# Kernel tuning notes

Hardware: AMD Instinct MI355X
Metric: run time of the kernel (lower is better)

## Reference

```python
import jax, jax.numpy as jnp
import numpy as np

N = 100000
NNZ = 3200000
NFEAT, NHID, NCLASS = 512, 256, 41

def setup_inputs() -> dict:
    key = jax.random.key(0)
    ks = jax.random.split(key, 8)
    x = jax.random.normal(ks[0], (N, NFEAT), dtype=jnp.float32)
    adj_rows = jnp.sort(jax.random.randint(ks[1], (NNZ,), 0, N))
    adj_cols = jax.random.randint(ks[2], (NNZ,), 0, N)
    adj_vals = jax.random.uniform(ks[3], (NNZ,), dtype=jnp.float32) / 32.0  # ~normalized adj
    s1 = 1.0 / np.sqrt(NHID)
    s2 = 1.0 / np.sqrt(NCLASS)
    w1 = jax.random.uniform(ks[4], (NFEAT, NHID), minval=-s1, maxval=s1, dtype=jnp.float32)
    b1 = jax.random.uniform(ks[5], (NHID,), minval=-s1, maxval=s1, dtype=jnp.float32)
    w2 = jax.random.uniform(ks[6], (NHID, NCLASS), minval=-s2, maxval=s2, dtype=jnp.float32)
    b2 = jax.random.uniform(ks[7], (NCLASS,), minval=-s2, maxval=s2, dtype=jnp.float32)
    return {"x": x, "adj_rows": adj_rows, "adj_cols": adj_cols, "adj_vals": adj_vals,
            "w1": w1, "b1": b1, "w2": w2, "b2": b2}

def spmm(rows, cols, vals, dense):
    # sparse [N,N] @ dense [N,D] via gather + segment_sum
    gathered = dense[cols] * vals[:, None]  # [nnz, D]
    return jax.ops.segment_sum(gathered, rows, num_segments=N)

def reference(x, adj_rows, adj_cols, adj_vals, w1, b1, w2, b2):
    # layer 1: A(XW) + b, relu  (GraphConvolution)
    h = spmm(adj_rows, adj_cols, adj_vals, x @ w1) + b1
    h = jax.nn.relu(h)
    # dropout: inference mode (training=False) -> identity
    # layer 2: (AX)W + b  (GraphConvolution2)
    out = spmm(adj_rows, adj_cols, adj_vals, h) @ w2 + b2
    return jax.nn.log_softmax(out, axis=1)
```

## Files before the change

kernel.cpp:

```cpp
#include <hip/hip_runtime.h>
#include <math.h>

#define N_NODES 100000
#define NNZ_E   3200000
#define NFEAT   512
#define NHID    256
#define NCLASS  41
#define NC_PAD  48
#define P_STRIDE 64

typedef __attribute__((ext_vector_type(8))) short   short8;
typedef __attribute__((ext_vector_type(8))) unsigned short ushort8;
typedef __attribute__((ext_vector_type(4))) float   f32x4;
typedef __attribute__((ext_vector_type(2))) float   f32x2;

__device__ __forceinline__ unsigned short f2bf(float f) {
    unsigned u = __builtin_bit_cast(unsigned, f);
    unsigned r = u + 0x7fffu + ((u >> 16) & 1u);
    return (unsigned short)(r >> 16);
}
__device__ __forceinline__ unsigned char f2fp8(float f) {
    return (unsigned char)(__builtin_amdgcn_cvt_pk_fp8_f32(f, 0.f, 0, false) & 0xff);
}

__global__ void prep_w_kernel(const float* __restrict__ w1, const float* __restrict__ w2,
                              unsigned short* __restrict__ w1t, unsigned short* __restrict__ w2t) {
    int tid = blockIdx.x * 256 + threadIdx.x;
    if (tid < NHID * NFEAT) {
        int n = tid >> 9, k = tid & 511;
        w1t[tid] = f2bf(w1[k * NHID + n]);
    }
    int t2 = tid - NHID * NFEAT;
    if (t2 >= 0 && t2 < NC_PAD * NHID) {
        int n = t2 >> 8, k = t2 & 255;
        w2t[t2] = (n < NCLASS) ? f2bf(w2[k * NCLASS + n]) : (unsigned short)0;
    }
}

__global__ void rowptr_kernel(const int* __restrict__ rows, int* __restrict__ row_ptr) {
    int r = blockIdx.x * 256 + threadIdx.x;
    if (r > N_NODES) return;
    int lo = 0, hi = NNZ_E;
    while (lo < hi) {
        int mid = (lo + hi) >> 1;
        if (rows[mid] < r) lo = mid + 1; else hi = mid;
    }
    row_ptr[r] = lo;
}

__global__ __launch_bounds__(256) void gemm1_kernel(const float* __restrict__ x,
                                                    const unsigned short* __restrict__ w1t,
                                                    unsigned char* __restrict__ xw) {
    const int rb   = blockIdx.x * 64;
    const int wave = threadIdx.x >> 6;
    const int lane = threadIdx.x & 63;
    const int l15  = lane & 15;
    const int quad = lane >> 4;

    f32x4 acc[4][4] = {};

    const float* arow_ptr[4];
#pragma unroll
    for (int mt = 0; mt < 4; mt++) {
        int r = rb + mt * 16 + l15;
        if (r >= N_NODES) r = N_NODES - 1;
        arow_ptr[mt] = x + (long)r * NFEAT + quad * 8;
    }
    const unsigned short* brow = w1t + (long)(wave * 64 + l15) * NFEAT + quad * 8;

    for (int kc = 0; kc < NFEAT; kc += 32) {
        short8 a[4];
#pragma unroll
        for (int mt = 0; mt < 4; mt++) {
            float4 f0 = *(const float4*)(arow_ptr[mt] + kc);
            float4 f1 = *(const float4*)(arow_ptr[mt] + kc + 4);
            ushort8 v;
            v[0] = f2bf(f0.x); v[1] = f2bf(f0.y); v[2] = f2bf(f0.z); v[3] = f2bf(f0.w);
            v[4] = f2bf(f1.x); v[5] = f2bf(f1.y); v[6] = f2bf(f1.z); v[7] = f2bf(f1.w);
            a[mt] = __builtin_bit_cast(short8, v);
        }
#pragma unroll
        for (int nt = 0; nt < 4; nt++) {
            short8 b = *(const short8*)(brow + (long)nt * 16 * NFEAT + kc);
#pragma unroll
            for (int mt = 0; mt < 4; mt++)
                acc[mt][nt] = __builtin_amdgcn_mfma_f32_16x16x32_bf16(a[mt], b, acc[mt][nt], 0, 0, 0);
        }
    }

#pragma unroll
    for (int mt = 0; mt < 4; mt++) {
#pragma unroll
        for (int nt = 0; nt < 4; nt++) {
            int col = wave * 64 + nt * 16 + l15;
#pragma unroll
            for (int r = 0; r < 4; r++) {
                int row = rb + mt * 16 + quad * 4 + r;
                if (row < N_NODES)
                    xw[(long)row * NHID + col] = f2fp8(acc[mt][nt][r]);
            }
        }
    }
}

__global__ __launch_bounds__(256) void spmm1_kernel(const unsigned char* __restrict__ xw,
                                                    const int* __restrict__ row_ptr,
                                                    const int* __restrict__ cols,
                                                    const float* __restrict__ vals,
                                                    const float* __restrict__ b1,
                                                    unsigned short* __restrict__ h) {
    int row = blockIdx.x * 4 + (threadIdx.x >> 6);
    if (row >= N_NODES) return;
    int lane = threadIdx.x & 63;
    int e0 = row_ptr[row], e1 = row_ptr[row + 1];

    float a0 = 0.f, a1 = 0.f, a2 = 0.f, a3 = 0.f;
    for (int base = e0; base < e1; base += 64) {
        int   myc = 0;
        float myv = 0.f;
        int idx = base + lane;
        if (idx < e1) { myc = cols[idx]; myv = vals[idx]; }
        int cnt = e1 - base; if (cnt > 64) cnt = 64;
        int j = 0;
        for (; j + 8 <= cnt; j += 8) {
            int c[8]; float v[8];
#pragma unroll
            for (int u = 0; u < 8; u++) { c[u] = __shfl(myc, j + u); v[u] = __shfl(myv, j + u); }
            unsigned q[8];
#pragma unroll
            for (int u = 0; u < 8; u++) q[u] = *(const unsigned*)(xw + (long)c[u] * NHID + lane * 4);
#pragma unroll
            for (int u = 0; u < 8; u++) {
                f32x2 lo = __builtin_amdgcn_cvt_pk_f32_fp8((int)q[u], false);
                f32x2 hi = __builtin_amdgcn_cvt_pk_f32_fp8((int)q[u], true);
                a0 += v[u] * lo[0];
                a1 += v[u] * lo[1];
                a2 += v[u] * hi[0];
                a3 += v[u] * hi[1];
            }
        }
        for (; j < cnt; j++) {
            int   c = __shfl(myc, j);
            float v = __shfl(myv, j);
            unsigned q = *(const unsigned*)(xw + (long)c * NHID + lane * 4);
            f32x2 lo = __builtin_amdgcn_cvt_pk_f32_fp8((int)q, false);
            f32x2 hi = __builtin_amdgcn_cvt_pk_f32_fp8((int)q, true);
            a0 += v * lo[0];
            a1 += v * lo[1];
            a2 += v * hi[0];
            a3 += v * hi[1];
        }
    }
    float4 bv = *(const float4*)(b1 + lane * 4);
    a0 = fmaxf(a0 + bv.x, 0.f);
    a1 = fmaxf(a1 + bv.y, 0.f);
    a2 = fmaxf(a2 + bv.z, 0.f);
    a3 = fmaxf(a3 + bv.w, 0.f);
    uint2 o;
    o.x = (unsigned)f2bf(a0) | ((unsigned)f2bf(a1) << 16);
    o.y = (unsigned)f2bf(a2) | ((unsigned)f2bf(a3) << 16);
    *(uint2*)(h + (long)row * NHID + lane * 4) = o;
}

__global__ __launch_bounds__(256) void gemm2_kernel(const unsigned short* __restrict__ h,
                                                    const unsigned short* __restrict__ w2t,
                                                    unsigned char* __restrict__ p) {
    int rt = blockIdx.x * 4 + (threadIdx.x >> 6);
    int row0 = rt * 16;
    if (row0 >= N_NODES) return;
    int lane = threadIdx.x & 63;
    int l15 = lane & 15, quad = lane >> 4;

    int arow = row0 + l15; if (arow >= N_NODES) arow = N_NODES - 1;
    f32x4 acc[3] = {};
#pragma unroll
    for (int kc = 0; kc < NHID; kc += 32) {
        short8 a = *(const short8*)(h + (long)arow * NHID + kc + quad * 8);
#pragma unroll
        for (int nt = 0; nt < 3; nt++) {
            short8 b = *(const short8*)(w2t + (long)(nt * 16 + l15) * NHID + kc + quad * 8);
            acc[nt] = __builtin_amdgcn_mfma_f32_16x16x32_bf16(a, b, acc[nt], 0, 0, 0);
        }
    }
#pragma unroll
    for (int nt = 0; nt < 3; nt++) {
        int col = nt * 16 + l15;
#pragma unroll
        for (int r = 0; r < 4; r++) {
            int row = row0 + quad * 4 + r;
            if (row < N_NODES)
                p[(long)row * P_STRIDE + col] = f2fp8(acc[nt][r]);
        }
    }
}

__global__ __launch_bounds__(256) void spmm2_kernel(const unsigned char* __restrict__ p,
                                                    const int* __restrict__ row_ptr,
                                                    const int* __restrict__ cols,
                                                    const float* __restrict__ vals,
                                                    const float* __restrict__ b2,
                                                    float* __restrict__ out) {
    int row = blockIdx.x * 4 + (threadIdx.x >> 6);
    if (row >= N_NODES) return;
    int lane = threadIdx.x & 63;
    int e = lane >> 5;
    int t = lane & 31;
    int e0 = row_ptr[row], e1 = row_ptr[row + 1];

    float a0 = 0.f, a1 = 0.f, a2 = 0.f, a3 = 0.f;
    for (int base = e0; base < e1; base += 64) {
        int   myc = 0;
        float myv = 0.f;
        int idx = base + lane;
        if (idx < e1) { myc = cols[idx]; myv = vals[idx]; }
        int cnt = e1 - base; if (cnt > 64) cnt = 64;
        int j = 0;
        for (; j + 8 <= cnt; j += 8) {
            int c[4]; float v[4];
#pragma unroll
            for (int u = 0; u < 4; u++) {
                c[u] = __shfl(myc, j + 2 * u + e);
                v[u] = __shfl(myv, j + 2 * u + e);
            }
            unsigned q[4];
#pragma unroll
            for (int u = 0; u < 4; u++)
                q[u] = (t < 12) ? *(const unsigned*)(p + (long)c[u] * P_STRIDE + 4 * t) : 0u;
#pragma unroll
            for (int u = 0; u < 4; u++) {
                f32x2 lo = __builtin_amdgcn_cvt_pk_f32_fp8((int)q[u], false);
                f32x2 hi = __builtin_amdgcn_cvt_pk_f32_fp8((int)q[u], true);
                a0 += v[u] * lo[0];
                a1 += v[u] * lo[1];
                a2 += v[u] * hi[0];
                a3 += v[u] * hi[1];
            }
        }
        for (; j < cnt; j += 2) {
            int jj = j + e;
            int jc = jj < cnt ? jj : cnt - 1;
            int   c = __shfl(myc, jc);
            float v = __shfl(myv, jc);
            if (jj >= cnt) v = 0.f;
            unsigned q = (t < 12) ? *(const unsigned*)(p + (long)c * P_STRIDE + 4 * t) : 0u;
            f32x2 lo = __builtin_amdgcn_cvt_pk_f32_fp8((int)q, false);
            f32x2 hi = __builtin_amdgcn_cvt_pk_f32_fp8((int)q, true);
            a0 += v * lo[0];
            a1 += v * lo[1];
            a2 += v * hi[0];
            a3 += v * hi[1];
        }
    }
    a0 += __shfl_xor(a0, 32);
    a1 += __shfl_xor(a1, 32);
    a2 += __shfl_xor(a2, 32);
    a3 += __shfl_xor(a3, 32);

    int c0 = 4 * t, c1 = 4 * t + 1, c2 = 4 * t + 2, c3 = 4 * t + 3;
    float l0 = (c0 < NCLASS) ? a0 + b2[c0] : -__builtin_inff();
    float l1 = (c1 < NCLASS) ? a1 + b2[c1] : -__builtin_inff();
    float l2 = (c2 < NCLASS) ? a2 + b2[c2] : -__builtin_inff();
    float l3 = (c3 < NCLASS) ? a3 + b2[c3] : -__builtin_inff();
    float m = fmaxf(fmaxf(l0, l1), fmaxf(l2, l3));
#pragma unroll
    for (int s = 16; s; s >>= 1) m = fmaxf(m, __shfl_xor(m, s));
    float esum = ((c0 < NCLASS) ? __expf(l0 - m) : 0.f)
               + ((c1 < NCLASS) ? __expf(l1 - m) : 0.f)
               + ((c2 < NCLASS) ? __expf(l2 - m) : 0.f)
               + ((c3 < NCLASS) ? __expf(l3 - m) : 0.f);
#pragma unroll
    for (int s = 16; s; s >>= 1) esum += __shfl_xor(esum, s);
    float lse = m + __logf(esum);
    if (e == 0) {
        long ob = (long)row * NCLASS;
        if (c0 < NCLASS) out[ob + c0] = l0 - lse;
        if (c1 < NCLASS) out[ob + c1] = l1 - lse;
        if (c2 < NCLASS) out[ob + c2] = l2 - lse;
        if (c3 < NCLASS) out[ob + c3] = l3 - lse;
    }
}

extern "C" void kernel_launch(void* const* d_in, const int* in_sizes, int n_in,
                              void* d_out, int out_size, void* d_ws, size_t ws_size,
                              hipStream_t stream) {
    const float* x        = (const float*)d_in[0];
    const int*   adj_rows = (const int*)  d_in[1];
    const int*   adj_cols = (const int*)  d_in[2];
    const float* adj_vals = (const float*)d_in[3];
    const float* w1       = (const float*)d_in[4];
    const float* b1       = (const float*)d_in[5];
    const float* w2       = (const float*)d_in[6];
    const float* b2       = (const float*)d_in[7];
    float* out = (float*)d_out;

    char* ws = (char*)d_ws;
    unsigned short* w1t     = (unsigned short*)(ws);
    unsigned short* w2t     = (unsigned short*)(ws + 0x40000);
    int*            row_ptr = (int*)           (ws + 0x46000);
    unsigned char*  xw      = (unsigned char*) (ws + 0xA8000);
    unsigned short* hbuf    = (unsigned short*)(ws + 0xA8000 + 25600000L);
    unsigned char*  p       = (unsigned char*) (ws + 0xA8000);

    prep_w_kernel<<<(NHID * NFEAT + NC_PAD * NHID + 255) / 256, 256, 0, stream>>>(w1, w2, w1t, w2t);
    rowptr_kernel<<<(N_NODES + 1 + 255) / 256, 256, 0, stream>>>(adj_rows, row_ptr);
    gemm1_kernel<<<(N_NODES + 63) / 64, 256, 0, stream>>>(x, w1t, xw);
    spmm1_kernel<<<(N_NODES + 3) / 4, 256, 0, stream>>>(xw, row_ptr, adj_cols, adj_vals, b1, hbuf);
    gemm2_kernel<<<((N_NODES + 15) / 16 + 3) / 4, 256, 0, stream>>>(hbuf, w2t, p);
    spmm2_kernel<<<(N_NODES + 3) / 4, 256, 0, stream>>>(p, row_ptr, adj_cols, adj_vals, b2, out);
}
```

Baseline: 634.3 us.

## Quantize x and W1 to FP8 and tile GEMM1 through LDS with FP8 MFMA

Adds a pre-pass that converts x to FP8 and stores W1 transposed as FP8. GEMM1 now uses 128x128 tiles staged through swizzled LDS with direct global-to-LDS loads, and FP8 MFMA in place of BF16. The goal is fewer bytes read in the GEMM and faster MFMA throughput. The trade-off is an extra full pass over x (read 200MB fp32, write 50MB), lower precision on the first-layer inputs, and a reshuffled workspace layout.

```diff
diff --git a/kernel.cpp b/kernel.cpp
--- a/kernel.cpp
+++ b/kernel.cpp
@@ -14,6 +14,9 @@
 typedef __attribute__((ext_vector_type(4))) float   f32x4;
 typedef __attribute__((ext_vector_type(2))) float   f32x2;
 
+typedef __attribute__((address_space(1))) const unsigned int gu32;
+typedef __attribute__((address_space(3))) unsigned int lu32;
+
 __device__ __forceinline__ unsigned short f2bf(float f) {
     unsigned u = __builtin_bit_cast(unsigned, f);
     unsigned r = u + 0x7fffu + ((u >> 16) & 1u);
@@ -23,12 +26,31 @@
     return (unsigned char)(__builtin_amdgcn_cvt_pk_fp8_f32(f, 0.f, 0, false) & 0xff);
 }
 
+__global__ __launch_bounds__(256) void prep_x_kernel(const float* __restrict__ x,
+                                                     unsigned char* __restrict__ xq) {
+    long i = (long)(blockIdx.x * 256 + threadIdx.x) * 16;
+    float4 f0 = *(const float4*)(x + i);
+    float4 f1 = *(const float4*)(x + i + 4);
+    float4 f2 = *(const float4*)(x + i + 8);
+    float4 f3 = *(const float4*)(x + i + 12);
+    uint4 o;
+    o.x = (unsigned)__builtin_amdgcn_cvt_pk_fp8_f32(f0.x, f0.y, 0, false);
+    o.x = (unsigned)__builtin_amdgcn_cvt_pk_fp8_f32(f0.z, f0.w, (int)o.x, true);
+    o.y = (unsigned)__builtin_amdgcn_cvt_pk_fp8_f32(f1.x, f1.y, 0, false);
+    o.y = (unsigned)__builtin_amdgcn_cvt_pk_fp8_f32(f1.z, f1.w, (int)o.y, true);
+    o.z = (unsigned)__builtin_amdgcn_cvt_pk_fp8_f32(f2.x, f2.y, 0, false);
+    o.z = (unsigned)__builtin_amdgcn_cvt_pk_fp8_f32(f2.z, f2.w, (int)o.z, true);
+    o.w = (unsigned)__builtin_amdgcn_cvt_pk_fp8_f32(f3.x, f3.y, 0, false);
+    o.w = (unsigned)__builtin_amdgcn_cvt_pk_fp8_f32(f3.z, f3.w, (int)o.w, true);
+    *(uint4*)(xq + i) = o;
+}
+
 __global__ void prep_w_kernel(const float* __restrict__ w1, const float* __restrict__ w2,
-                              unsigned short* __restrict__ w1t, unsigned short* __restrict__ w2t) {
+                              unsigned char* __restrict__ w1q, unsigned short* __restrict__ w2t) {
     int tid = blockIdx.x * 256 + threadIdx.x;
     if (tid < NHID * NFEAT) {
         int n = tid >> 9, k = tid & 511;
-        w1t[tid] = f2bf(w1[k * NHID + n]);
+        w1q[tid] = f2fp8(w1[k * NHID + n]);
     }
     int t2 = tid - NHID * NFEAT;
     if (t2 >= 0 && t2 < NC_PAD * NHID) {
@@ -48,54 +70,78 @@
     row_ptr[r] = lo;
 }
 
-__global__ __launch_bounds__(256) void gemm1_kernel(const float* __restrict__ x,
-                                                    const unsigned short* __restrict__ w1t,
+__global__ __launch_bounds__(256) void gemm1_kernel(const unsigned char* __restrict__ xq,
+                                                    const unsigned char* __restrict__ w1q,
                                                     unsigned char* __restrict__ xw) {
-    const int rb   = blockIdx.x * 64;
-    const int wave = threadIdx.x >> 6;
+    __shared__ unsigned char As[8192];
+    __shared__ unsigned char Bs[8192];
+
+    const int wv   = threadIdx.x >> 6;
     const int lane = threadIdx.x & 63;
     const int l15  = lane & 15;
     const int quad = lane >> 4;
+    const int rb   = blockIdx.x * 128;
+    const int nb   = blockIdx.y * 128;
+
+    const int srow0 = (wv * 2 + 0) * 16 + (lane >> 2);
+    const int srow1 = (wv * 2 + 1) * 16 + (lane >> 2);
+    const int g0 = (lane & 3) ^ ((srow0 >> 1) & 3);
+    const int g1 = (lane & 3) ^ ((srow1 >> 1) & 3);
+    int ga0 = rb + srow0; if (ga0 >= N_NODES) ga0 = N_NODES - 1;
+    int ga1 = rb + srow1; if (ga1 >= N_NODES) ga1 = N_NODES - 1;
+    const unsigned char* agp0 = xq + (long)ga0 * NFEAT + g0 * 16;
+    const unsigned char* agp1 = xq + (long)ga1 * NFEAT + g1 * 16;
+    const unsigned char* bgp0 = w1q + (long)(nb + srow0) * NFEAT + g0 * 16;
+    const unsigned char* bgp1 = w1q + (long)(nb + srow1) * NFEAT + g1 * 16;
 
     f32x4 acc[4][4] = {};
 
-    const float* arow_ptr[4];
+    for (int kc = 0; kc < NFEAT; kc += 64) {
+        __builtin_amdgcn_global_load_lds((gu32*)(agp0 + kc), (lu32*)(As + (wv * 2 + 0) * 1024), 16, 0, 0);
+        __builtin_amdgcn_global_load_lds((gu32*)(agp1 + kc), (lu32*)(As + (wv * 2 + 1) * 1024), 16, 0, 0);
+        __builtin_amdgcn_global_load_lds((gu32*)(bgp0 + kc), (lu32*)(Bs + (wv * 2 + 0) * 1024), 16, 0, 0);
+        __builtin_amdgcn_global_load_lds((gu32*)(bgp1 + kc), (lu32*)(Bs + (wv * 2 + 1) * 1024), 16, 0, 0);
+        __syncthreads();
+
+        unsigned long long a[4][2], b[4][2];
+#pragma unroll
+        for (int mt = 0; mt < 4; mt++) {
+            int row = (wv & 1) * 64 + mt * 16 + l15;
+#pragma unroll
+            for (int ks = 0; ks < 2; ks++) {
+                int p8 = (ks * 4 + quad) ^ (row & 6);
+                a[mt][ks] = *(const unsigned long long*)(As + row * 64 + p8 * 8);
+            }
+        }
+#pragma unroll
+        for (int nt = 0; nt < 4; nt++) {
+            int nr = (wv >> 1) * 64 + nt * 16 + l15;
+#pragma unroll
+            for (int ks = 0; ks < 2; ks++) {
+                int p8 = (ks * 4 + quad) ^ (nr & 6);
+                b[nt][ks] = *(const unsigned long long*)(Bs + nr * 64 + p8 * 8);
+            }
+        }
+#pragma unroll
+        for (int ks = 0; ks < 2; ks++)
+#pragma unroll
+            for (int nt = 0; nt < 4; nt++)
+#pragma unroll
+                for (int mt = 0; mt < 4; mt++)
+                    acc[mt][nt] = __builtin_amdgcn_mfma_f32_16x16x32_fp8_fp8(
+                        (long)a[mt][ks], (long)b[nt][ks], acc[mt][nt], 0, 0, 0);
+        __syncthreads();
+    }
+
 #pragma unroll
     for (int mt = 0; mt < 4; mt++) {
-        int r = rb + mt * 16 + l15;
-        if (r >= N_NODES) r = N_NODES - 1;
-        arow_ptr[mt] = x + (long)r * NFEAT + quad * 8;
-    }
-    const unsigned short* brow = w1t + (long)(wave * 64 + l15) * NFEAT + quad * 8;
-
-    for (int kc = 0; kc < NFEAT; kc += 32) {
-        short8 a[4];
-#pragma unroll
-        for (int mt = 0; mt < 4; mt++) {
-            float4 f0 = *(const float4*)(arow_ptr[mt] + kc);
-            float4 f1 = *(const float4*)(arow_ptr[mt] + kc + 4);
-            ushort8 v;
-            v[0] = f2bf(f0.x); v[1] = f2bf(f0.y); v[2] = f2bf(f0.z); v[3] = f2bf(f0.w);
-            v[4] = f2bf(f1.x); v[5] = f2bf(f1.y); v[6] = f2bf(f1.z); v[7] = f2bf(f1.w);
-            a[mt] = __builtin_bit_cast(short8, v);
-        }
+        int row0 = rb + (wv & 1) * 64 + mt * 16 + quad * 4;
 #pragma unroll
         for (int nt = 0; nt < 4; nt++) {
-            short8 b = *(const short8*)(brow + (long)nt * 16 * NFEAT + kc);
-#pragma unroll
-            for (int mt = 0; mt < 4; mt++)
-                acc[mt][nt] = __builtin_amdgcn_mfma_f32_16x16x32_bf16(a[mt], b, acc[mt][nt], 0, 0, 0);
-        }
-    }
-
-#pragma unroll
-    for (int mt = 0; mt < 4; mt++) {
-#pragma unroll
-        for (int nt = 0; nt < 4; nt++) {
-            int col = wave * 64 + nt * 16 + l15;
+            int col = nb + (wv >> 1) * 64 + nt * 16 + l15;
 #pragma unroll
             for (int r = 0; r < 4; r++) {
-                int row = rb + mt * 16 + quad * 4 + r;
+                int row = row0 + r;
                 if (row < N_NODES)
                     xw[(long)row * NHID + col] = f2fp8(acc[mt][nt][r]);
             }
@@ -294,16 +340,18 @@
     float* out = (float*)d_out;
 
     char* ws = (char*)d_ws;
-    unsigned short* w1t     = (unsigned short*)(ws);
-    unsigned short* w2t     = (unsigned short*)(ws + 0x40000);
-    int*            row_ptr = (int*)           (ws + 0x46000);
-    unsigned char*  xw      = (unsigned char*) (ws + 0xA8000);
-    unsigned short* hbuf    = (unsigned short*)(ws + 0xA8000 + 25600000L);
-    unsigned char*  p       = (unsigned char*) (ws + 0xA8000);
-
-    prep_w_kernel<<<(NHID * NFEAT + NC_PAD * NHID + 255) / 256, 256, 0, stream>>>(w1, w2, w1t, w2t);
+    unsigned char*  w1q     = (unsigned char*) (ws);
+    unsigned short* w2t     = (unsigned short*)(ws + 0x20000);
+    int*            row_ptr = (int*)           (ws + 0x26000);
+    unsigned char*  xq      = (unsigned char*) (ws + 0x90000);
+    unsigned short* hbuf    = (unsigned short*)(ws + 0x90000);
+    unsigned char*  xw      = (unsigned char*) (ws + 0x3180000);
+    unsigned char*  p       = (unsigned char*) (ws + 0x3180000);
+
+    prep_x_kernel<<<(N_NODES * NFEAT) / 16 / 256, 256, 0, stream>>>(x, xq);
+    prep_w_kernel<<<(NHID * NFEAT + NC_PAD * NHID + 255) / 256, 256, 0, stream>>>(w1, w2, w1q, w2t);
     rowptr_kernel<<<(N_NODES + 1 + 255) / 256, 256, 0, stream>>>(adj_rows, row_ptr);
-    gemm1_kernel<<<(N_NODES + 63) / 64, 256, 0, stream>>>(x, w1t, xw);
+    gemm1_kernel<<<dim3((N_NODES + 127) / 128, 2), 256, 0, stream>>>(xq, w1q, xw);
     spmm1_kernel<<<(N_NODES + 3) / 4, 256, 0, stream>>>(xw, row_ptr, adj_cols, adj_vals, b1, hbuf);
     gemm2_kernel<<<((N_NODES + 15) / 16 + 3) / 4, 256, 0, stream>>>(hbuf, w2t, p);
     spmm2_kernel<<<(N_NODES + 3) / 4, 256, 0, stream>>>(p, row_ptr, adj_cols, adj_vals, b2, out);
```

Result: faster. 570.0 us (-10.1%).
